# Performance work log

Hardware: AMD Instinct MI355X
Metric: run time of the kernel (lower is better)

Reference implementation:

```python
import jax, jax.numpy as jnp
import numpy as np

D_MODEL = 1024
NUM_HEADS = 16
DILATION_RATE = 4
SEGMENT_SIZE = 512
BATCH = 4
SEQ_LEN = 8192


def setup_inputs() -> dict:
    key = jax.random.key(0)
    k_x, k_wqkv, k_wo = jax.random.split(key, 3)
    x = jax.random.normal(k_x, (BATCH, SEQ_LEN, D_MODEL), dtype=jnp.float32)
    # Per-dilation-branch FlashMHA params (fused QKV proj + out proj), stacked.
    Wqkv = jax.random.normal(k_wqkv, (DILATION_RATE, 3 * D_MODEL, D_MODEL), dtype=jnp.float32) * 0.02
    bqkv = jnp.zeros((DILATION_RATE, 3 * D_MODEL), dtype=jnp.float32)
    Wo = jax.random.normal(k_wo, (DILATION_RATE, D_MODEL, D_MODEL), dtype=jnp.float32) * 0.02
    bo = jnp.zeros((DILATION_RATE, D_MODEL), dtype=jnp.float32)
    return {"x": x, "Wqkv": Wqkv, "bqkv": bqkv, "Wo": Wo, "bo": bo}


def _branch(x, Wqkv_i, bqkv_i, Wo_i, bo_i, offset):
    """One dilation branch: strided gather -> segmented MHA -> scatter back."""
    B, S, D = x.shape
    hd = D // NUM_HEADS
    x_ = x[:, offset::DILATION_RATE, :]                      # [B, S/r, D]
    n_seg = x_.shape[1] // SEGMENT_SIZE
    x_ = x_.reshape(B, n_seg, SEGMENT_SIZE, D)               # [B, n, s, D]
    qkv = jnp.einsum('bnsd,ed->bnse', x_, Wqkv_i) + bqkv_i   # [B, n, s, 3D]
    q, k, v = jnp.split(qkv, 3, axis=-1)
    q = q.reshape(B, n_seg, SEGMENT_SIZE, NUM_HEADS, hd)
    k = k.reshape(B, n_seg, SEGMENT_SIZE, NUM_HEADS, hd)
    v = v.reshape(B, n_seg, SEGMENT_SIZE, NUM_HEADS, hd)
    scores = jnp.einsum('bnqhd,bnkhd->bnhqk', q, k) / jnp.sqrt(jnp.asarray(hd, q.dtype))
    attn = jax.nn.softmax(scores, axis=-1)
    o = jnp.einsum('bnhqk,bnkhd->bnqhd', attn, v).reshape(B, n_seg, SEGMENT_SIZE, D)
    o = jnp.einsum('bnsd,ed->bnse', o, Wo_i) + bo_i          # out projection
    full = jnp.zeros((B, S, D), x.dtype).at[:, offset::DILATION_RATE, :].set(
        o.reshape(B, -1, D))
    return full


def reference(x, Wqkv, bqkv, Wo, bo):
    outs = [
        _branch(x, Wqkv[i], bqkv[i], Wo[i], bo[i], offset=i % DILATION_RATE)
        for i in range(DILATION_RATE)
    ]
    # softmax over uniform logits -> equal weights, kept for faithfulness
    weights = jax.nn.softmax(jnp.full((DILATION_RATE,), 1.0 / DILATION_RATE, dtype=x.dtype))
    out = outs[0] * weights[0]
    for i in range(1, DILATION_RATE):
        out = out + weights[i] * outs[i]
    return out
```

## Files before the change

### kernel.cpp

```cpp
#include <hip/hip_runtime.h>
#include <hip/hip_bf16.h>


typedef __bf16 bf16_t;
typedef __bf16 bf16x8 __attribute__((ext_vector_type(8)));
typedef __bf16 bf16x4 __attribute__((ext_vector_type(4)));
typedef float  f32x4  __attribute__((ext_vector_type(4)));

typedef __attribute__((address_space(1))) void gvoid;
typedef __attribute__((address_space(3))) void lvoid;

__device__ __forceinline__ void gload16(const void* g, void* l) {
  __builtin_amdgcn_global_load_lds((gvoid*)g, (lvoid*)l, 16, 0, 0);
}

#define MFMA16(a, b, c) __builtin_amdgcn_mfma_f32_16x16x32_bf16((a), (b), (c), 0, 0, 0)

#define BARRIER()  asm volatile("s_barrier" ::: "memory")
#define WAITLGKM0() do { asm volatile("s_waitcnt lgkmcnt(0)" ::: "memory"); \
                         __builtin_amdgcn_sched_barrier(0); } while (0)

__global__ void cvt3_f32_bf16(const float* __restrict__ x, const float* __restrict__ wq,
                              const float* __restrict__ wo, bf16_t* __restrict__ xb,
                              bf16_t* __restrict__ wqb, bf16_t* __restrict__ wob) {
  const int NX = 33554432, NWQ = 12582912, NWO = 4194304;
  const int NTOT = NX + NWQ + NWO;
  int i = (blockIdx.x * blockDim.x + threadIdx.x) * 8;
  int stride = gridDim.x * blockDim.x * 8;
  for (; i < NTOT; i += stride) {
    const float* src; bf16_t* dst; int off;
    if (i < NX)            { src = x;  dst = xb;  off = i; }
    else if (i < NX + NWQ) { src = wq; dst = wqb; off = i - NX; }
    else                   { src = wo; dst = wob; off = i - NX - NWQ; }
    float4 u = *(const float4*)(src + off);
    float4 v = *(const float4*)(src + off + 4);
    bf16x8 o;
    o[0] = (bf16_t)u.x; o[1] = (bf16_t)u.y; o[2] = (bf16_t)u.z; o[3] = (bf16_t)u.w;
    o[4] = (bf16_t)v.x; o[5] = (bf16_t)v.y; o[6] = (bf16_t)v.z; o[7] = (bf16_t)v.w;
    *(bf16x8*)(dst + off) = o;
  }
}


#define As ((bf16_t(*)[2][128][64])SHM)
#define Bs ((bf16_t(*)[2][128][64])(SHM + 32768))
#define Cs ((bf16_t(*)[256])SHM)

#define GEMM8_DECLS()                                                          \
  __shared__ __align__(16) bf16_t SHM[65536];                                  \
  const int tid = threadIdx.x;                                                 \
  const int l = tid & 63, wid = tid >> 6;                                      \
  const int wr = wid >> 2, wc = wid & 3;                                       \
  const int rl = l & 15, rq = l >> 4;                                          \
  const int trow = tid >> 3;                                                   \
  const size_t swcol = ((size_t)((tid & 7) ^ (trow & 7))) << 3;                \
  f32x4 acc[8][4];                                                             \
  bf16x8 aq[4][2], aqB[4][2], bq0[2][2], bq1[2][2];

#define ACC_ZERO()                                                             \
  _Pragma("unroll") for (int m = 0; m < 8; ++m)                                \
    _Pragma("unroll") for (int n = 0; n < 4; ++n)                              \
      acc[m][n] = (f32x4){0.f, 0.f, 0.f, 0.f};

#define LD_AQX(cur, mh, dst)                                                   \
  do {                                                                         \
    _Pragma("unroll") for (int j = 0; j < 4; ++j)                              \
      _Pragma("unroll") for (int kk = 0; kk < 2; ++kk) {                       \
        int R_ = (mh)*64 + j*16 + rl;                                          \
        int C_ = (kk*32 + rq*8) ^ ((rl & 7) << 3);                             \
        dst[j][kk] = *(const bf16x8*)&As[cur][wr][R_][C_];                     \
      }                                                                        \
  } while (0)

#define LD_BQ(cur, nh, dst)                                                    \
  do {                                                                         \
    _Pragma("unroll") for (int i = 0; i < 2; ++i)                              \
      _Pragma("unroll") for (int kk = 0; kk < 2; ++kk) {                       \
        int R_ = (wc & 1)*64 + ((nh)*2 + i)*16 + rl;                           \
        int C_ = (kk*32 + rq*8) ^ ((rl & 7) << 3);                             \
        dst[i][kk] = *(const bf16x8*)&Bs[cur][wc >> 1][R_][C_];                \
      }                                                                        \
  } while (0)

#define MF_QX(mh, nh, A_, B_)                                                  \
  do {                                                                         \
    __builtin_amdgcn_s_setprio(1);                                             \
    _Pragma("unroll") for (int j = 0; j < 4; ++j)                              \
      _Pragma("unroll") for (int i = 0; i < 2; ++i) {                          \
        acc[(mh)*4+j][(nh)*2+i] = MFMA16(A_[j][0], B_[i][0], acc[(mh)*4+j][(nh)*2+i]); \
        acc[(mh)*4+j][(nh)*2+i] = MFMA16(A_[j][1], B_[i][1], acc[(mh)*4+j][(nh)*2+i]); \
      }                                                                        \
    __builtin_amdgcn_s_setprio(0);                                             \
  } while (0)

#define ST_A(k2, half)                                                         \
  do { if ((k2) < 16) {                                                        \
    bf16_t* d_ = &As[(k2) & 1][half][0][0];                                    \
    gload16(aSrc + (size_t)((half)*128) * ARSTRIDE + (size_t)(k2)*64, d_ + tid*8);          \
    gload16(aSrc + (size_t)((half)*128 + 64) * ARSTRIDE + (size_t)(k2)*64, d_ + 4096 + tid*8); } \
  } while (0)

#define ST_B(k2, half)                                                         \
  do { if ((k2) < 16) {                                                        \
    bf16_t* d_ = &Bs[(k2) & 1][half][0][0];                                    \
    gload16(bSrc + (size_t)((half)*128) * 1024 + (size_t)(k2)*64, d_ + tid*8);              \
    gload16(bSrc + (size_t)((half)*128 + 64) * 1024 + (size_t)(k2)*64, d_ + 4096 + tid*8); } \
  } while (0)

#define GEMM8_MAINLOOP_R10()                                                   \
  ST_A(0, 0); ST_A(0, 1); ST_B(0, 0); ST_B(0, 1);                              \
  ST_B(1, 0); ST_B(1, 1); ST_A(1, 0);                                          \
  asm volatile("s_waitcnt vmcnt(6)" ::: "memory");                             \
  BARRIER();                                                                   \
  LD_AQX(0, 0, aq);                                                            \
  _Pragma("unroll 2")                                                          \
  for (int kt = 0; kt < 16; ++kt) {                                            \
    const int cur = kt & 1;                                                    \
                                                                      \
    LD_BQ(cur, 0, bq0);                                                        \
    ST_A(kt + 1, 1);                                                           \
    BARRIER(); WAITLGKM0();                                                    \
    MF_QX(0, 0, aq, bq0);                                                      \
    BARRIER();                                                                 \
                                                                      \
    LD_BQ(cur, 1, bq1);                                                        \
    ST_B(kt + 2, 0);                                                           \
    BARRIER(); WAITLGKM0();                                                    \
    MF_QX(0, 1, aq, bq1);                                                      \
    BARRIER();                                                                 \
                                                                      \
    LD_AQX(cur, 1, aqB);                                                       \
    ST_B(kt + 2, 1);                                                           \
    BARRIER(); WAITLGKM0();                                                    \
    MF_QX(1, 1, aqB, bq1);                                                     \
    BARRIER();                                                                 \
                                                                      \
    ST_A(kt + 2, 0);                                                           \
    if (kt < 14) asm volatile("s_waitcnt vmcnt(6)" ::: "memory");              \
    else         asm volatile("s_waitcnt vmcnt(0)" ::: "memory");              \
    BARRIER();                                                                 \
    if (kt < 15) { LD_AQX(cur ^ 1, 0, aq); }     \
    MF_QX(1, 0, aqB, bq0);                                                     \
    BARRIER();                                                                 \
  }

__launch_bounds__(512, 2)
__global__ void qkv_gemm8(const bf16_t* __restrict__ xb, const bf16_t* __restrict__ wb,
                          const float* __restrict__ bqkv,
                          bf16_t* __restrict__ qbuf, bf16_t* __restrict__ kbuf,
                          bf16_t* __restrict__ vbuf) {
  GEMM8_DECLS();
  ACC_ZERO();
  const int flat = blockIdx.y * 12 + blockIdx.x;
  const int nb = (flat & 7) * 192 + (flat >> 3);
  const int ntile = nb % 12, mtile = nb / 12;
  const int br = (mtile >> 3) & 3;
  const int b0 = mtile >> 5, seg0 = (mtile >> 1) & 3, s00 = (mtile & 1) * 256;
  const int xrow_base = (b0 << 13) + br + ((seg0 << 9) + s00) * 4;

#define ARSTRIDE 4096
  const bf16_t* aSrc = xb + (size_t)(xrow_base + 4 * trow) * 1024 + swcol;
  const bf16_t* bSrc = wb + ((size_t)br * 3072 + ntile * 256 + trow) * 1024 + swcol;

  GEMM8_MAINLOOP_R10();
#undef ARSTRIDE

  const int part = ntile >> 2;
  const int sb = (b0 * 4 + br) * 4 + seg0;
  const float scale = (part == 0) ? 0.125f : 1.0f;

#pragma unroll
  for (int m = 0; m < 8; ++m) {
    int t_loc = wr * 128 + m * 16 + rq * 4;
#pragma unroll
    for (int n = 0; n < 4; ++n) {
      int e_loc = wc * 64 + n * 16 + rl;
      float bias = bqkv[br * 3072 + ntile * 256 + e_loc];
      if (part != 2) {
#pragma unroll
        for (int r = 0; r < 4; ++r) {
          int t = t_loc + r;
          Cs[t][e_loc ^ ((t & 7) << 3)] = (bf16_t)((acc[m][n][r] + bias) * scale);
        }
      } else {
        bf16x4 pk;
#pragma unroll
        for (int r = 0; r < 4; ++r) pk[r] = (bf16_t)(acc[m][n][r] + bias);
        *(bf16x4*)&Cs[e_loc][t_loc ^ ((e_loc & 7) << 3)] = pk;
      }
    }
  }
  __syncthreads();

  if (part != 2) {
    bf16_t* dst0 = (part == 0) ? qbuf : kbuf;
    const int hbase = (part == 0) ? ntile * 4 : (ntile - 4) * 4;
    const int lane8 = tid & 7;
#pragma unroll
    for (int it = 0; it < 16; ++it) {
      int R = it * 64 + (tid >> 3);
      int h2 = R >> 8, t = R & 255;
      int e_loc = h2 * 64 + lane8 * 8;
      bf16x8 v = *(const bf16x8*)&Cs[t][e_loc ^ ((t & 7) << 3)];
      size_t bh = (size_t)sb * 16 + hbase + h2;
      *(bf16x8*)&dst0[(bh * 512 + s00 + t) * 64 + lane8 * 8] = v;
    }
  } else {
    const int hbase = (ntile - 8) * 4;
    const int lane32 = tid & 31;
#pragma unroll
    for (int it = 0; it < 16; ++it) {
      int row_e = it * 16 + (tid >> 5);
      int t0 = lane32 * 8;
      bf16x8 v = *(const bf16x8*)&Cs[row_e][t0 ^ ((row_e & 7) << 3)];
      size_t bh = (size_t)sb * 16 + hbase + (row_e >> 6);
      int dh = row_e & 63;
      *(bf16x8*)&vbuf[(bh * 64 + dh) * 512 + s00 + t0] = v;
    }
  }
}

__launch_bounds__(512, 2)
__global__ void proj_gemm8(const bf16_t* __restrict__ ob, const bf16_t* __restrict__ wob,
                           const float* __restrict__ bo, float* __restrict__ out) {
  GEMM8_DECLS();
  ACC_ZERO();
  const int flat = blockIdx.y * 4 + blockIdx.x;
  const int nb = (flat & 7) * 64 + (flat >> 3);
  const int ntile = nb & 3, mtile = nb >> 2;
  const int br = (mtile >> 3) & 3;
  const int b0 = mtile >> 5, seg0 = (mtile >> 1) & 3, s00 = (mtile & 1) * 256;

#define ARSTRIDE 1024
  const bf16_t* aSrc = ob + (size_t)(mtile * 256 + trow) * 1024 + swcol;
  const bf16_t* bSrc = wob + ((size_t)br * 1024 + ntile * 256 + trow) * 1024 + swcol;

  GEMM8_MAINLOOP_R10();
#undef ARSTRIDE

  float* CsF = (float*)SHM;
  const int col0 = (l & 63) * 4;
#pragma unroll
  for (int H = 0; H < 2; ++H) {
    __syncthreads();
    if (wr == H) {
#pragma unroll
      for (int n = 0; n < 4; ++n) {
        int col = wc * 64 + n * 16 + rl;
        float bias = bo[br * 1024 + ntile * 256 + col];
#pragma unroll
        for (int m = 0; m < 8; ++m) {
#pragma unroll
          for (int r = 0; r < 4; ++r) {
            int tl = m * 16 + rq * 4 + r;
            int pc = col ^ (((tl >> 2) & 7) << 2);
            CsF[tl * 256 + pc] = 0.25f * (acc[m][n][r] + bias);
          }
        }
      }
    }
    __syncthreads();
#pragma unroll
    for (int it = 0; it < 16; ++it) {
      int tl = it * 8 + wid;
      int pc = col0 ^ (((tl >> 2) & 7) << 2);
      float4 v = *(const float4*)&CsF[tl * 256 + pc];
      int t = br + (((seg0 << 9) + s00 + H * 128 + tl) << 2);
      *(float4*)&out[((size_t)b0 * 8192 + t) * 1024 + ntile * 256 + col0] = v;
    }
  }
}

__launch_bounds__(256, 4)
__global__ void attn_kernel(const bf16_t* __restrict__ qb, const bf16_t* __restrict__ kb,
                            const bf16_t* __restrict__ vb, bf16_t* __restrict__ ob) {
  __shared__ bf16_t QPs[64][64];
  __shared__ bf16_t Ks[2][64][64];
  __shared__ bf16_t VTs[2][64][64];
  const int tid = threadIdx.x, l = tid & 63, w = tid >> 6;

  const int flat = blockIdx.y * 8 + blockIdx.x;
  const int nb = (flat & 7) * 1024 + (flat >> 3);
  const int qblk = nb & 7;
  const int bh = nb >> 3;

  const int srow = tid >> 3;
  const int scol = (((tid & 7) ^ (srow & 7)) << 3);

  const bf16_t* qsrc = qb + (size_t)bh * 32768 + qblk * 4096;
  gload16(qsrc + srow * 64 + scol, &QPs[0][0] + tid * 8);
  gload16(qsrc + 2048 + srow * 64 + scol, &QPs[0][0] + 2048 + tid * 8);

  const bf16_t* kbase = kb + (size_t)bh * 32768;
  const bf16_t* vbase = vb + (size_t)bh * 32768;

  gload16(kbase + srow * 64 + scol, &Ks[0][0][0] + tid * 8);
  gload16(kbase + 2048 + srow * 64 + scol, &Ks[0][0][0] + 2048 + tid * 8);
  gload16(vbase + (size_t)srow * 512 + scol, &VTs[0][0][0] + tid * 8);
  gload16(vbase + (size_t)(srow + 32) * 512 + scol, &VTs[0][0][0] + 2048 + tid * 8);

  float lsum[4];
  f32x4 accO[4];
#pragma unroll
  for (int r = 0; r < 4; ++r) lsum[r] = 0.f;
#pragma unroll
  for (int di = 0; di < 4; ++di) accO[di] = (f32x4){0.f, 0.f, 0.f, 0.f};

  __syncthreads();

  bf16x8 aq[2];
#pragma unroll
  for (int kk = 0; kk < 2; ++kk) {
    int R = w * 16 + (l & 15);
    int C = (kk * 32 + (l >> 4) * 8) ^ ((R & 7) << 3);
    aq[kk] = *(bf16x8*)&QPs[R][C];
  }

  int cur = 0;
  for (int kt = 0; kt < 8; ++kt) {
    if (kt < 7) {
      int nxt = cur ^ 1;
      gload16(kbase + (kt + 1) * 4096 + srow * 64 + scol, &Ks[nxt][0][0] + tid * 8);
      gload16(kbase + (kt + 1) * 4096 + 2048 + srow * 64 + scol, &Ks[nxt][0][0] + 2048 + tid * 8);
      gload16(vbase + (size_t)srow * 512 + (kt + 1) * 64 + scol, &VTs[nxt][0][0] + tid * 8);
      gload16(vbase + (size_t)(srow + 32) * 512 + (kt + 1) * 64 + scol,
              &VTs[nxt][0][0] + 2048 + tid * 8);
    }

    f32x4 sf[4];
#pragma unroll
    for (int ni = 0; ni < 4; ++ni) sf[ni] = (f32x4){0.f, 0.f, 0.f, 0.f};
#pragma unroll
    for (int kk = 0; kk < 2; ++kk) {
#pragma unroll
      for (int ni = 0; ni < 4; ++ni) {
        int R = ni * 16 + (l & 15);
        int C = (kk * 32 + (l >> 4) * 8) ^ ((R & 7) << 3);
        bf16x8 bk = *(bf16x8*)&Ks[cur][R][C];
        sf[ni] = MFMA16(aq[kk], bk, sf[ni]);
      }
    }

#pragma unroll
    for (int ni = 0; ni < 4; ++ni)
#pragma unroll
      for (int r = 0; r < 4; ++r) {
        float p = __expf(sf[ni][r]);
        sf[ni][r] = p;
        lsum[r] += p;
      }

#pragma unroll
    for (int ni = 0; ni < 4; ++ni)
#pragma unroll
      for (int r = 0; r < 4; ++r) {
        int Rp = w * 16 + ((l >> 4) << 2) + r;
        int Cp = (ni * 16 + (l & 15)) ^ ((Rp & 7) << 3);
        QPs[Rp][Cp] = (bf16_t)sf[ni][r];
      }
    WAITLGKM0();

#pragma unroll
    for (int kk = 0; kk < 2; ++kk) {
      int Rp = w * 16 + (l & 15);
      int Cp = (kk * 32 + (l >> 4) * 8) ^ ((Rp & 7) << 3);
      bf16x8 apv = *(bf16x8*)&QPs[Rp][Cp];
#pragma unroll
      for (int di = 0; di < 4; ++di) {
        int R = di * 16 + (l & 15);
        int C = (kk * 32 + (l >> 4) * 8) ^ ((R & 7) << 3);
        bf16x8 bv = *(bf16x8*)&VTs[cur][R][C];
        accO[di] = MFMA16(apv, bv, accO[di]);
      }
    }
    __syncthreads();
    cur ^= 1;
  }

#pragma unroll
  for (int r = 0; r < 4; ++r) {
#pragma unroll
    for (int off = 1; off < 16; off <<= 1) lsum[r] += __shfl_xor(lsum[r], off);
  }

  bf16_t(*Ob)[72] = (bf16_t(*)[72])(&Ks[0][0][0]);
#pragma unroll
  for (int r = 0; r < 4; ++r) {
    float inv = 1.f / lsum[r];
    int row = w * 16 + ((l >> 4) << 2) + r;
#pragma unroll
    for (int di = 0; di < 4; ++di)
      Ob[row][di * 16 + (l & 15)] = (bf16_t)(accO[di][r] * inv);
  }
  WAITLGKM0();

  const int tok0 = (bh >> 4) * 512 + qblk * 64;
  const int h = bh & 15;
#pragma unroll
  for (int it = 0; it < 2; ++it) {
    int rloc = w * 16 + it * 8 + (l >> 3);
    bf16x8 v = *(const bf16x8*)&Ob[rloc][(l & 7) * 8];
    *(bf16x8*)&ob[(size_t)(tok0 + rloc) * 1024 + h * 64 + (l & 7) * 8] = v;
  }
}

extern "C" void kernel_launch(void* const* d_in, const int* in_sizes, int n_in,
                              void* d_out, int out_size, void* d_ws, size_t ws_size,
                              hipStream_t stream) {
  const float* x    = (const float*)d_in[0];
  const float* Wqkv = (const float*)d_in[1];
  const float* bqkv = (const float*)d_in[2];
  const float* Wo   = (const float*)d_in[3];
  const float* bo   = (const float*)d_in[4];
  float* out = (float*)d_out;

  const int NX  = 4 * 8192 * 1024;
  const int NWQ = 4 * 3072 * 1024;
  const int NWO = 4 * 1024 * 1024;
  const int NT  = 32768 * 1024;

  bf16_t* xb   = (bf16_t*)d_ws;
  bf16_t* wqb  = xb + NX;
  bf16_t* wob  = wqb + NWQ;
  bf16_t* qbuf = wob + NWO;
  bf16_t* kbuf = qbuf + NT;
  bf16_t* vbuf = kbuf + NT;
  bf16_t* obuf = xb;

  cvt3_f32_bf16<<<2048, 256, 0, stream>>>(x, Wqkv, Wo, xb, wqb, wob);

  qkv_gemm8<<<dim3(12, 128), 512, 0, stream>>>(xb, wqb, bqkv, qbuf, kbuf, vbuf);
  attn_kernel<<<dim3(8, 1024), 256, 0, stream>>>(qbuf, kbuf, vbuf, obuf);
  proj_gemm8<<<dim3(4, 128), 512, 0, stream>>>(obuf, wob, bo, out);
}
```

Baseline: 470.3 us.

## Process two query blocks per attention workgroup to reuse K/V tiles

```diff
diff --git a/kernel.cpp b/kernel.cpp
--- a/kernel.cpp
+++ b/kernel.cpp
@@ -279,41 +279,54 @@
   __shared__ bf16_t VTs[2][64][64];
   const int tid = threadIdx.x, l = tid & 63, w = tid >> 6;
 
-  const int flat = blockIdx.y * 8 + blockIdx.x;
-  const int nb = (flat & 7) * 1024 + (flat >> 3);
-  const int qblk = nb & 7;
-  const int bh = nb >> 3;
+  const int flat = blockIdx.y * 4 + blockIdx.x;
+  const int nb = (flat & 7) * 512 + (flat >> 3);
+  const int qblk2 = nb & 3;
+  const int bh = nb >> 2;
 
   const int srow = tid >> 3;
   const int scol = (((tid & 7) ^ (srow & 7)) << 3);
 
-  const bf16_t* qsrc = qb + (size_t)bh * 32768 + qblk * 4096;
+  const bf16_t* qsrc = qb + (size_t)bh * 32768 + qblk2 * 8192;
+  const bf16_t* kbase = kb + (size_t)bh * 32768;
+  const bf16_t* vbase = vb + (size_t)bh * 32768;
+
   gload16(qsrc + srow * 64 + scol, &QPs[0][0] + tid * 8);
   gload16(qsrc + 2048 + srow * 64 + scol, &QPs[0][0] + 2048 + tid * 8);
-
-  const bf16_t* kbase = kb + (size_t)bh * 32768;
-  const bf16_t* vbase = vb + (size_t)bh * 32768;
-
   gload16(kbase + srow * 64 + scol, &Ks[0][0][0] + tid * 8);
   gload16(kbase + 2048 + srow * 64 + scol, &Ks[0][0][0] + 2048 + tid * 8);
   gload16(vbase + (size_t)srow * 512 + scol, &VTs[0][0][0] + tid * 8);
   gload16(vbase + (size_t)(srow + 32) * 512 + scol, &VTs[0][0][0] + 2048 + tid * 8);
 
-  float lsum[4];
-  f32x4 accO[4];
-#pragma unroll
-  for (int r = 0; r < 4; ++r) lsum[r] = 0.f;
-#pragma unroll
-  for (int di = 0; di < 4; ++di) accO[di] = (f32x4){0.f, 0.f, 0.f, 0.f};
+  float lsum[2][4];
+  f32x4 accO[2][4];
+#pragma unroll
+  for (int h = 0; h < 2; ++h) {
+#pragma unroll
+    for (int r = 0; r < 4; ++r) lsum[h][r] = 0.f;
+#pragma unroll
+    for (int di = 0; di < 4; ++di) accO[h][di] = (f32x4){0.f, 0.f, 0.f, 0.f};
+  }
 
   __syncthreads();
 
-  bf16x8 aq[2];
+  bf16x8 aq[2][2];
 #pragma unroll
   for (int kk = 0; kk < 2; ++kk) {
     int R = w * 16 + (l & 15);
     int C = (kk * 32 + (l >> 4) * 8) ^ ((R & 7) << 3);
-    aq[kk] = *(bf16x8*)&QPs[R][C];
+    aq[0][kk] = *(bf16x8*)&QPs[R][C];
+  }
+  __syncthreads();
+
+  gload16(qsrc + 4096 + srow * 64 + scol, &QPs[0][0] + tid * 8);
+  gload16(qsrc + 6144 + srow * 64 + scol, &QPs[0][0] + 2048 + tid * 8);
+  __syncthreads();
+#pragma unroll
+  for (int kk = 0; kk < 2; ++kk) {
+    int R = w * 16 + (l & 15);
+    int C = (kk * 32 + (l >> 4) * 8) ^ ((R & 7) << 3);
+    aq[1][kk] = *(bf16x8*)&QPs[R][C];
   }
 
   int cur = 0;
@@ -327,80 +340,85 @@
               &VTs[nxt][0][0] + 2048 + tid * 8);
     }
 
-    f32x4 sf[4];
-#pragma unroll
-    for (int ni = 0; ni < 4; ++ni) sf[ni] = (f32x4){0.f, 0.f, 0.f, 0.f};
-#pragma unroll
-    for (int kk = 0; kk < 2; ++kk) {
-#pragma unroll
-      for (int ni = 0; ni < 4; ++ni) {
-        int R = ni * 16 + (l & 15);
-        int C = (kk * 32 + (l >> 4) * 8) ^ ((R & 7) << 3);
-        bf16x8 bk = *(bf16x8*)&Ks[cur][R][C];
-        sf[ni] = MFMA16(aq[kk], bk, sf[ni]);
+#pragma unroll
+    for (int h = 0; h < 2; ++h) {
+      f32x4 sf[4];
+#pragma unroll
+      for (int ni = 0; ni < 4; ++ni) sf[ni] = (f32x4){0.f, 0.f, 0.f, 0.f};
+#pragma unroll
+      for (int kk = 0; kk < 2; ++kk) {
+#pragma unroll
+        for (int ni = 0; ni < 4; ++ni) {
+          int R = ni * 16 + (l & 15);
+          int C = (kk * 32 + (l >> 4) * 8) ^ ((R & 7) << 3);
+          bf16x8 bk = *(bf16x8*)&Ks[cur][R][C];
+          sf[ni] = MFMA16(aq[h][kk], bk, sf[ni]);
+        }
       }
-    }
-
-#pragma unroll
-    for (int ni = 0; ni < 4; ++ni)
-#pragma unroll
-      for (int r = 0; r < 4; ++r) {
-        float p = __expf(sf[ni][r]);
-        sf[ni][r] = p;
-        lsum[r] += p;
-      }
-
-#pragma unroll
-    for (int ni = 0; ni < 4; ++ni)
-#pragma unroll
-      for (int r = 0; r < 4; ++r) {
-        int Rp = w * 16 + ((l >> 4) << 2) + r;
-        int Cp = (ni * 16 + (l & 15)) ^ ((Rp & 7) << 3);
-        QPs[Rp][Cp] = (bf16_t)sf[ni][r];
-      }
-    WAITLGKM0();
-
-#pragma unroll
-    for (int kk = 0; kk < 2; ++kk) {
-      int Rp = w * 16 + (l & 15);
-      int Cp = (kk * 32 + (l >> 4) * 8) ^ ((Rp & 7) << 3);
-      bf16x8 apv = *(bf16x8*)&QPs[Rp][Cp];
-#pragma unroll
-      for (int di = 0; di < 4; ++di) {
-        int R = di * 16 + (l & 15);
-        int C = (kk * 32 + (l >> 4) * 8) ^ ((R & 7) << 3);
-        bf16x8 bv = *(bf16x8*)&VTs[cur][R][C];
-        accO[di] = MFMA16(apv, bv, accO[di]);
+
+#pragma unroll
+      for (int ni = 0; ni < 4; ++ni)
+#pragma unroll
+        for (int r = 0; r < 4; ++r) {
+          float p = __expf(sf[ni][r]);
+          sf[ni][r] = p;
+          lsum[h][r] += p;
+        }
+
+#pragma unroll
+      for (int ni = 0; ni < 4; ++ni)
+#pragma unroll
+        for (int r = 0; r < 4; ++r) {
+          int Rp = w * 16 + ((l >> 4) << 2) + r;
+          int Cp = (ni * 16 + (l & 15)) ^ ((Rp & 7) << 3);
+          QPs[Rp][Cp] = (bf16_t)sf[ni][r];
+        }
+      WAITLGKM0();
+
+#pragma unroll
+      for (int kk = 0; kk < 2; ++kk) {
+        int Rp = w * 16 + (l & 15);
+        int Cp = (kk * 32 + (l >> 4) * 8) ^ ((Rp & 7) << 3);
+        bf16x8 apv = *(bf16x8*)&QPs[Rp][Cp];
+#pragma unroll
+        for (int di = 0; di < 4; ++di) {
+          int R = di * 16 + (l & 15);
+          int C = (kk * 32 + (l >> 4) * 8) ^ ((R & 7) << 3);
+          bf16x8 bv = *(bf16x8*)&VTs[cur][R][C];
+          accO[h][di] = MFMA16(apv, bv, accO[h][di]);
+        }
       }
     }
     __syncthreads();
     cur ^= 1;
   }
 
-#pragma unroll
-  for (int r = 0; r < 4; ++r) {
-#pragma unroll
-    for (int off = 1; off < 16; off <<= 1) lsum[r] += __shfl_xor(lsum[r], off);
-  }
-
   bf16_t(*Ob)[72] = (bf16_t(*)[72])(&Ks[0][0][0]);
-#pragma unroll
-  for (int r = 0; r < 4; ++r) {
-    float inv = 1.f / lsum[r];
-    int row = w * 16 + ((l >> 4) << 2) + r;
-#pragma unroll
-    for (int di = 0; di < 4; ++di)
-      Ob[row][di * 16 + (l & 15)] = (bf16_t)(accO[di][r] * inv);
-  }
-  WAITLGKM0();
-
-  const int tok0 = (bh >> 4) * 512 + qblk * 64;
+  const int tok0 = (bh >> 4) * 512 + qblk2 * 128;
   const int h = bh & 15;
 #pragma unroll
-  for (int it = 0; it < 2; ++it) {
-    int rloc = w * 16 + it * 8 + (l >> 3);
-    bf16x8 v = *(const bf16x8*)&Ob[rloc][(l & 7) * 8];
-    *(bf16x8*)&ob[(size_t)(tok0 + rloc) * 1024 + h * 64 + (l & 7) * 8] = v;
+  for (int qh = 0; qh < 2; ++qh) {
+#pragma unroll
+    for (int r = 0; r < 4; ++r) {
+#pragma unroll
+      for (int off = 1; off < 16; off <<= 1)
+        lsum[qh][r] += __shfl_xor(lsum[qh][r], off);
+    }
+#pragma unroll
+    for (int r = 0; r < 4; ++r) {
+      float inv = 1.f / lsum[qh][r];
+      int row = w * 16 + ((l >> 4) << 2) + r;
+#pragma unroll
+      for (int di = 0; di < 4; ++di)
+        Ob[row][di * 16 + (l & 15)] = (bf16_t)(accO[qh][di][r] * inv);
+    }
+    WAITLGKM0();
+#pragma unroll
+    for (int it = 0; it < 2; ++it) {
+      int rloc = w * 16 + it * 8 + (l >> 3);
+      bf16x8 v = *(const bf16x8*)&Ob[rloc][(l & 7) * 8];
+      *(bf16x8*)&ob[(size_t)(tok0 + qh * 64 + rloc) * 1024 + h * 64 + (l & 7) * 8] = v;
+    }
   }
 }
 
@@ -430,6 +448,6 @@
   cvt3_f32_bf16<<<2048, 256, 0, stream>>>(x, Wqkv, Wo, xb, wqb, wob);
 
   qkv_gemm8<<<dim3(12, 128), 512, 0, stream>>>(xb, wqb, bqkv, qbuf, kbuf, vbuf);
-  attn_kernel<<<dim3(8, 1024), 256, 0, stream>>>(qbuf, kbuf, vbuf, obuf);
+  attn_kernel<<<dim3(4, 1024), 256, 0, stream>>>(qbuf, kbuf, vbuf, obuf);
   proj_gemm8<<<dim3(4, 128), 512, 0, stream>>>(obuf, wob, bo, out);
 }
```

After: 459.0 us (median of 2 runs). 2.4% less time.
